# Kernel optimization log

Hardware: AMD Instinct MI355X
Metric: run time of the kernel (lower is better)

The kernel has to match this reference:

```python
import jax, jax.numpy as jnp
import numpy as np

B, S, HIDDEN = 4, 2048, 1024
NUM_EXPERTS = 8
TOP_K = 4
EPS = 1e-6


def setup_inputs() -> dict:
    key = jax.random.key(0)
    k0, k1, k2 = jax.random.split(key, 3)
    x = jax.random.normal(k0, (B, S, HIDDEN), dtype=jnp.float32)
    Wg = jax.random.normal(k1, (HIDDEN, NUM_EXPERTS), dtype=jnp.float32) * 0.02
    bg = jnp.zeros((NUM_EXPERTS,), dtype=jnp.float32)
    W = jax.random.normal(k2, (NUM_EXPERTS, HIDDEN, HIDDEN), dtype=jnp.float32) * 0.02
    b = jnp.zeros((NUM_EXPERTS, HIDDEN), dtype=jnp.float32)
    return {"x": x, "Wg": Wg, "bg": bg, "W": W, "b": b}


def reference(x, Wg, bg, W, b):
    Bb, Ss, D = x.shape
    xf = x.reshape(-1, D)                       # [T, D]
    T = xf.shape[0]

    # --- router ---
    router_logits = xf @ Wg + bg                # [T, E]
    router_probs = jax.nn.softmax(router_logits, axis=-1)
    top_k_probs, top_k_indices = jax.lax.top_k(router_probs, TOP_K)  # [T, K]
    top_k_weights = top_k_probs / (top_k_probs.sum(axis=-1, keepdims=True) + EPS)
    expert_mask = jax.nn.one_hot(top_k_indices, NUM_EXPERTS, dtype=jnp.float32).sum(axis=1)  # [T, E]

    # --- experts: original computes every expert on every token then masks;
    # same math expressed as one batched GEMM + gather ---
    all_out = jnp.einsum('td,edf->etf', xf, W) + b[:, None, :]  # [E, T, D]
    sel = all_out[top_k_indices.T, jnp.arange(T)[None, :]]      # [K, T, D]
    moe_output = jnp.einsum('tk,ktd->td', top_k_weights, sel).reshape(Bb, Ss, D)

    # --- load-balancing aux loss ---
    aux_loss = jnp.dot(expert_mask.mean(axis=0), router_probs.mean(axis=0)) * NUM_EXPERTS
    return moe_output, aux_loss
```

## Files before the change

kernel.cpp:

```cpp
#include <hip/hip_runtime.h>
#include <hip/hip_bf16.h>

#define T_TOK 8192
#define DH    1024
#define NE    8
#define TK    4

typedef unsigned short u16;
typedef __bf16 bf16x8 __attribute__((ext_vector_type(8)));
typedef float  f32x4  __attribute__((ext_vector_type(4)));

__device__ __forceinline__ u16 f2b(float f) {
    union { float f; unsigned u; } v; v.f = f;
    unsigned u = v.u;
    u += 0x7FFFu + ((u >> 16) & 1u);
    return (u16)(u >> 16);
}
__device__ __forceinline__ float b2f(u16 h) {
    union { unsigned u; float f; } v; v.u = ((unsigned)h) << 16;
    return v.f;
}
__device__ __forceinline__ void glds16(const u16* g, u16* l) {
    __builtin_amdgcn_global_load_lds((const __attribute__((address_space(1))) void*)g,
                                     (__attribute__((address_space(3))) void*)l, 16, 0, 0);
}

__global__ __launch_bounds__(256) void cast_w_kernel(const float* __restrict__ W,
                                                     u16* __restrict__ wbt) {
    __shared__ float tile[64][65];
    const int e  = blockIdx.z;
    const int d0 = blockIdx.y * 64;
    const int f0 = blockIdx.x * 64;
    const int r  = threadIdx.x >> 4;
    const int c4 = (threadIdx.x & 15) * 4;
    const float* src = W + ((size_t)e << 20) + (size_t)d0 * DH + f0;
    #pragma unroll
    for (int i = 0; i < 4; i++) {
        const int row = i * 16 + r;
        const float4 v = *(const float4*)(src + (size_t)row * DH + c4);
        tile[row][c4]     = v.x;
        tile[row][c4 + 1] = v.y;
        tile[row][c4 + 2] = v.z;
        tile[row][c4 + 3] = v.w;
    }
    __syncthreads();
    u16* dst = wbt + ((size_t)e << 20) + (size_t)f0 * DH + d0;
    #pragma unroll
    for (int i = 0; i < 4; i++) {
        const int orow = i * 16 + r;
        ushort4 o;
        o.x = f2b(tile[c4][orow]);
        o.y = f2b(tile[c4 + 1][orow]);
        o.z = f2b(tile[c4 + 2][orow]);
        o.w = f2b(tile[c4 + 3][orow]);
        *(ushort4*)(dst + (size_t)orow * DH + c4) = o;
    }
}

__global__ __launch_bounds__(512) void router_kernel(
    const float* __restrict__ x, const float* __restrict__ Wg, const float* __restrict__ bg,
    u16* __restrict__ xb,
    int* __restrict__ bucket_tok, float* __restrict__ bucket_w,
    int* __restrict__ tk_e, float* __restrict__ tk_w,
    int* __restrict__ cnt, float* __restrict__ probsum)
{
    __shared__ int   lcnt[NE];
    __shared__ float lprob[NE];
    __shared__ int   gbase[NE];
    const int tid = threadIdx.x;
    const int wv = tid >> 6, lane = tid & 63;
    const int t = blockIdx.x * 8 + wv;
    if (tid < NE) { lcnt[tid] = 0; lprob[tid] = 0.f; }
    __syncthreads();

    float a[NE] = {};
    {
        const float* xr = x + (size_t)t * DH;
        u16* xbr = xb + (size_t)t * DH;
        #pragma unroll
        for (int it = 0; it < 4; it++) {
            const int d = it * 256 + lane * 4;
            const float4 v = *(const float4*)(xr + d);
            ushort4 o;
            o.x = f2b(v.x); o.y = f2b(v.y); o.z = f2b(v.z); o.w = f2b(v.w);
            *(ushort4*)(xbr + d) = o;
            const float* wr = Wg + d * NE;
            #pragma unroll
            for (int e = 0; e < NE; e++)
                a[e] += v.x * wr[e] + v.y * wr[NE + e] + v.z * wr[2 * NE + e] + v.w * wr[3 * NE + e];
        }
    }
    #pragma unroll
    for (int e = 0; e < NE; e++) {
        float v = a[e];
        #pragma unroll
        for (int off = 32; off > 0; off >>= 1) v += __shfl_down(v, off);
        a[e] = v;
    }

    int idx4[TK]; float w4[TK]; int off4[TK];
    if (lane == 0) {
        float logits[NE], probs[NE];
        float mx = -1e30f;
        #pragma unroll
        for (int e = 0; e < NE; e++) { logits[e] = a[e] + bg[e]; mx = fmaxf(mx, logits[e]); }
        float Z = 0.f;
        #pragma unroll
        for (int e = 0; e < NE; e++) { probs[e] = expf(logits[e] - mx); Z += probs[e]; }
        const float rZ = 1.f / Z;
        #pragma unroll
        for (int e = 0; e < NE; e++) probs[e] *= rZ;

        float rem2[NE];
        #pragma unroll
        for (int e = 0; e < NE; e++) rem2[e] = probs[e];
        float s4 = 0.f;
        #pragma unroll
        for (int k = 0; k < TK; k++) {
            int best = 0; float bv = rem2[0];
            #pragma unroll
            for (int e = 1; e < NE; e++) if (rem2[e] > bv) { bv = rem2[e]; best = e; }
            idx4[k] = best; w4[k] = bv; s4 += bv; rem2[best] = -1e30f;
        }
        const float rs = 1.f / (s4 + 1e-6f);
        #pragma unroll
        for (int k = 0; k < TK; k++) {
            w4[k] *= rs;
            tk_e[t * TK + k] = idx4[k];
            tk_w[t * TK + k] = w4[k];
            off4[k] = atomicAdd(&lcnt[idx4[k]], 1);
        }
        #pragma unroll
        for (int e = 0; e < NE; e++) atomicAdd(&lprob[e], probs[e]);
    }
    __syncthreads();
    if (tid < NE) {
        gbase[tid] = atomicAdd(&cnt[tid], lcnt[tid]);
        atomicAdd(&probsum[tid], lprob[tid]);
    }
    __syncthreads();
    if (lane == 0) {
        #pragma unroll
        for (int k = 0; k < TK; k++) {
            const int e = idx4[k];
            const int slot = gbase[e] + off4[k];
            bucket_tok[e * T_TOK + slot] = (t << 2) | k;
            bucket_w[e * T_TOK + slot]   = w4[k];
        }
    }
}

__global__ __launch_bounds__(256) void moe_gemm_kernel(
    const u16* __restrict__ xb, const u16* __restrict__ wbt,
    const int* __restrict__ bucket_tok, const float* __restrict__ bucket_w,
    const int* __restrict__ cnt, u16* __restrict__ y)
{
    const int e  = blockIdx.z;
    const int M  = cnt[e];
    const int m0 = blockIdx.y * 128;
    if (m0 >= M) return;
    const int n0 = blockIdx.x * 128;

    __shared__ u16 As[128 * 32];
    __shared__ u16 Bs[128 * 32];
    __shared__ int   s_tok[128];
    __shared__ float s_w[128];

    const int tid  = threadIdx.x;
    const int lane = tid & 63;
    const int wave = tid >> 6;

    if (tid < 128) {
        const int slot = m0 + tid;
        if (slot < M) {
            s_tok[tid] = bucket_tok[e * T_TOK + slot];
            s_w[tid]   = bucket_w[e * T_TOK + slot];
        } else { s_tok[tid] = -1; s_w[tid] = 0.f; }
    }
    __syncthreads();

    const int l4 = lane >> 2;
    const int c8 = (lane & 3) * 8;
    const int r0 = (2 * wave) * 16 + l4;
    const int r1 = r0 + 16;
    const int t0 = s_tok[r0], t1 = s_tok[r1];
    const u16* gA0 = xb + (size_t)(t0 >= 0 ? (t0 >> 2) : 0) * DH + c8;
    const u16* gA1 = xb + (size_t)(t1 >= 0 ? (t1 >> 2) : 0) * DH + c8;
    const u16* gB0 = wbt + ((size_t)e << 20) + (size_t)(n0 + r0) * DH + c8;
    const u16* gB1 = gB0 + (size_t)16 * DH;
    u16* lA0 = &As[(2 * wave)     * 512];
    u16* lA1 = &As[(2 * wave + 1) * 512];
    u16* lB0 = &Bs[(2 * wave)     * 512];
    u16* lB1 = &Bs[(2 * wave + 1) * 512];

    const int mrow = (wave >> 1) * 64;
    const int ncol = (wave & 1) * 64;
    const int fr   = lane & 15;
    const int fq   = (lane >> 4) * 8;

    f32x4 acc[4][4] = {};

    for (int k0 = 0; k0 < DH; k0 += 32) {
        glds16(gA0 + k0, lA0);
        glds16(gA1 + k0, lA1);
        glds16(gB0 + k0, lB0);
        glds16(gB1 + k0, lB1);
        __syncthreads();
        bf16x8 af[4], bfv[4];
        #pragma unroll
        for (int i = 0; i < 4; i++)
            af[i] = *(const bf16x8*)&As[(mrow + i * 16 + fr) * 32 + fq];
        #pragma unroll
        for (int j = 0; j < 4; j++)
            bfv[j] = *(const bf16x8*)&Bs[(ncol + j * 16 + fr) * 32 + fq];
        #pragma unroll
        for (int i = 0; i < 4; i++)
            #pragma unroll
            for (int j = 0; j < 4; j++)
                acc[i][j] = __builtin_amdgcn_mfma_f32_16x16x32_bf16(af[i], bfv[j], acc[i][j], 0, 0, 0);
        __syncthreads();
    }

    const int cl = lane & 15;
    const int rb = (lane >> 4) * 4;
    #pragma unroll
    for (int i = 0; i < 4; i++) {
        #pragma unroll
        for (int r = 0; r < 4; r++) {
            const int srow = mrow + i * 16 + rb + r;
            const int tok = s_tok[srow];
            if (tok < 0) continue;
            const float w = s_w[srow];
            u16* yr = y + (size_t)tok * DH + (n0 + ncol + cl);
            #pragma unroll
            for (int j = 0; j < 4; j++)
                yr[j * 16] = f2b(acc[i][j][r] * w);
        }
    }
}

__global__ __launch_bounds__(256) void combine_kernel(
    const u16* __restrict__ y, const int* __restrict__ tk_e, const float* __restrict__ tk_w,
    const float* __restrict__ bexp,
    const int* __restrict__ cnt, const float* __restrict__ probsum,
    float* __restrict__ out, float* __restrict__ out_aux)
{
    const int t = blockIdx.x;
    const int c = threadIdx.x * 4;
    if (t == 0 && threadIdx.x == 0) {
        float s = 0.f;
        for (int e = 0; e < NE; e++) s += (float)cnt[e] * probsum[e];
        out_aux[0] = s * (float)NE / ((float)T_TOK * (float)T_TOK);
    }
    float o0 = 0.f, o1 = 0.f, o2 = 0.f, o3 = 0.f;
    #pragma unroll
    for (int k = 0; k < TK; k++) {
        const int e   = tk_e[t * TK + k];
        const float w = tk_w[t * TK + k];
        const ushort4 yv = *(const ushort4*)(y + ((size_t)(t * TK + k)) * DH + c);
        const float4  bv = *(const float4*)(bexp + (size_t)e * DH + c);
        o0 += b2f(yv.x) + w * bv.x;
        o1 += b2f(yv.y) + w * bv.y;
        o2 += b2f(yv.z) + w * bv.z;
        o3 += b2f(yv.w) + w * bv.w;
    }
    float4 ov = {o0, o1, o2, o3};
    *(float4*)(out + (size_t)t * DH + c) = ov;
}

extern "C" void kernel_launch(void* const* d_in, const int* in_sizes, int n_in,
                              void* d_out, int out_size, void* d_ws, size_t ws_size,
                              hipStream_t stream)
{
    const float* x  = (const float*)d_in[0];
    const float* Wg = (const float*)d_in[1];
    const float* bg = (const float*)d_in[2];
    const float* W  = (const float*)d_in[3];
    const float* b  = (const float*)d_in[4];
    float* out = (float*)d_out;

    char* ws = (char*)d_ws;
    u16*   xb         = (u16*)(ws);
    u16*   wbt        = (u16*)(ws + 16777216);
    u16*   y          = (u16*)(ws + 33554432);
    int*   bucket_tok = (int*)(ws + 100663296);
    float* bucket_w   = (float*)(ws + 100925440);
    int*   tk_e       = (int*)(ws + 101187584);
    float* tk_w       = (float*)(ws + 101318656);
    int*   cnt        = (int*)(ws + 101449728);
    float* probsum    = (float*)(ws + 101449760);

    hipMemsetAsync(cnt, 0, 64, stream);

    cast_w_kernel<<<dim3(16, 16, NE), 256, 0, stream>>>(W, wbt);
    router_kernel<<<1024, 512, 0, stream>>>(x, Wg, bg, xb, bucket_tok, bucket_w, tk_e, tk_w, cnt, probsum);
    moe_gemm_kernel<<<dim3(8, 64, NE), 256, 0, stream>>>(xb, wbt, bucket_tok, bucket_w, cnt, y);
    combine_kernel<<<8192, 256, 0, stream>>>(y, tk_e, tk_w, b, cnt, probsum, out, out + (size_t)T_TOK * DH);
}
```

Before: 259.8 us.

## Double-buffer LDS tiles in MoE GEMM with async prefetch two stages ahead

```diff
diff --git a/kernel.cpp b/kernel.cpp
--- a/kernel.cpp
+++ b/kernel.cpp
@@ -24,6 +24,9 @@
     __builtin_amdgcn_global_load_lds((const __attribute__((address_space(1))) void*)g,
                                      (__attribute__((address_space(3))) void*)l, 16, 0, 0);
 }
+
+#define FENCE() asm volatile("" ::: "memory")
+#define SBAR()  do { FENCE(); __builtin_amdgcn_s_barrier(); FENCE(); } while (0)
 
 __global__ __launch_bounds__(256) void cast_w_kernel(const float* __restrict__ W,
                                                      u16* __restrict__ wbt) {
@@ -161,8 +164,8 @@
     if (m0 >= M) return;
     const int n0 = blockIdx.x * 128;
 
-    __shared__ u16 As[128 * 32];
-    __shared__ u16 Bs[128 * 32];
+    __shared__ u16 As[2][128 * 32];
+    __shared__ u16 Bs[2][128 * 32];
     __shared__ int   s_tok[128];
     __shared__ float s_w[128];
 
@@ -188,10 +191,7 @@
     const u16* gA1 = xb + (size_t)(t1 >= 0 ? (t1 >> 2) : 0) * DH + c8;
     const u16* gB0 = wbt + ((size_t)e << 20) + (size_t)(n0 + r0) * DH + c8;
     const u16* gB1 = gB0 + (size_t)16 * DH;
-    u16* lA0 = &As[(2 * wave)     * 512];
-    u16* lA1 = &As[(2 * wave + 1) * 512];
-    u16* lB0 = &Bs[(2 * wave)     * 512];
-    u16* lB1 = &Bs[(2 * wave + 1) * 512];
+    const int chunk = (2 * wave) * 512;
 
     const int mrow = (wave >> 1) * 64;
     const int ncol = (wave & 1) * 64;
@@ -200,25 +200,39 @@
 
     f32x4 acc[4][4] = {};
 
-    for (int k0 = 0; k0 < DH; k0 += 32) {
-        glds16(gA0 + k0, lA0);
-        glds16(gA1 + k0, lA1);
-        glds16(gB0 + k0, lB0);
-        glds16(gB1 + k0, lB1);
-        __syncthreads();
+    auto stage = [&](int kt) {
+        const int b  = kt & 1;
+        const int ko = kt * 32;
+        glds16(gA0 + ko, &As[b][chunk]);
+        glds16(gA1 + ko, &As[b][chunk + 512]);
+        glds16(gB0 + ko, &Bs[b][chunk]);
+        glds16(gB1 + ko, &Bs[b][chunk + 512]);
+    };
+
+    stage(0); stage(1);
+    asm volatile("s_waitcnt vmcnt(4)" ::: "memory");
+    SBAR();
+
+    for (int t = 0; t < 32; ++t) {
+        const int b = t & 1;
         bf16x8 af[4], bfv[4];
         #pragma unroll
         for (int i = 0; i < 4; i++)
-            af[i] = *(const bf16x8*)&As[(mrow + i * 16 + fr) * 32 + fq];
+            af[i] = *(const bf16x8*)&As[b][(mrow + i * 16 + fr) * 32 + fq];
         #pragma unroll
         for (int j = 0; j < 4; j++)
-            bfv[j] = *(const bf16x8*)&Bs[(ncol + j * 16 + fr) * 32 + fq];
+            bfv[j] = *(const bf16x8*)&Bs[b][(ncol + j * 16 + fr) * 32 + fq];
+        asm volatile("s_waitcnt lgkmcnt(0)" ::: "memory");
+        SBAR();
+        if (t + 2 < 32) stage(t + 2);
         #pragma unroll
         for (int i = 0; i < 4; i++)
             #pragma unroll
             for (int j = 0; j < 4; j++)
                 acc[i][j] = __builtin_amdgcn_mfma_f32_16x16x32_bf16(af[i], bfv[j], acc[i][j], 0, 0, 0);
-        __syncthreads();
+        if (t < 30)       asm volatile("s_waitcnt vmcnt(4)" ::: "memory");
+        else if (t == 30) asm volatile("s_waitcnt vmcnt(0)" ::: "memory");
+        if (t < 31) SBAR();
     }
 
     const int cl = lane & 15;
```

New measurement: 259.2 us. About the same (-0.3%).

## Rewrite expert GEMM as persistent 256x256 double-buffered swizzled pipeline

Applied to the files above, without the earlier changes.

```diff
diff --git a/kernel.cpp b/kernel.cpp
--- a/kernel.cpp
+++ b/kernel.cpp
@@ -24,6 +24,11 @@
     __builtin_amdgcn_global_load_lds((const __attribute__((address_space(1))) void*)g,
                                      (__attribute__((address_space(3))) void*)l, 16, 0, 0);
 }
+
+#define FENCE() asm volatile("" ::: "memory")
+#define SBAR()  do { FENCE(); __builtin_amdgcn_s_barrier(); FENCE(); } while (0)
+#define WAITLGKM0() do { asm volatile("s_waitcnt lgkmcnt(0)" ::: "memory"); \
+                         __builtin_amdgcn_sched_barrier(0); } while (0)
 
 __global__ __launch_bounds__(256) void cast_w_kernel(const float* __restrict__ W,
                                                      u16* __restrict__ wbt) {
@@ -150,91 +155,170 @@
     }
 }
 
-__global__ __launch_bounds__(256) void moe_gemm_kernel(
+__global__ __launch_bounds__(512, 2) void moe_gemm_kernel(
     const u16* __restrict__ xb, const u16* __restrict__ wbt,
     const int* __restrict__ bucket_tok, const float* __restrict__ bucket_w,
     const int* __restrict__ cnt, u16* __restrict__ y)
 {
-    const int e  = blockIdx.z;
-    const int M  = cnt[e];
-    const int m0 = blockIdx.y * 128;
-    if (m0 >= M) return;
-    const int n0 = blockIdx.x * 128;
-
-    __shared__ u16 As[128 * 32];
-    __shared__ u16 Bs[128 * 32];
-    __shared__ int   s_tok[128];
-    __shared__ float s_w[128];
+    __shared__ u16 As[2][256 * 64];
+    __shared__ u16 Bs[2][256 * 64];
+    __shared__ int   s_tok[256];
+    __shared__ float s_w[256];
 
     const int tid  = threadIdx.x;
     const int lane = tid & 63;
-    const int wave = tid >> 6;
-
-    if (tid < 128) {
-        const int slot = m0 + tid;
-        if (slot < M) {
-            s_tok[tid] = bucket_tok[e * T_TOK + slot];
-            s_w[tid]   = bucket_w[e * T_TOK + slot];
-        } else { s_tok[tid] = -1; s_w[tid] = 0.f; }
-    }
-    __syncthreads();
-
-    const int l4 = lane >> 2;
-    const int c8 = (lane & 3) * 8;
-    const int r0 = (2 * wave) * 16 + l4;
-    const int r1 = r0 + 16;
-    const int t0 = s_tok[r0], t1 = s_tok[r1];
-    const u16* gA0 = xb + (size_t)(t0 >= 0 ? (t0 >> 2) : 0) * DH + c8;
-    const u16* gA1 = xb + (size_t)(t1 >= 0 ? (t1 >> 2) : 0) * DH + c8;
-    const u16* gB0 = wbt + ((size_t)e << 20) + (size_t)(n0 + r0) * DH + c8;
-    const u16* gB1 = gB0 + (size_t)16 * DH;
-    u16* lA0 = &As[(2 * wave)     * 512];
-    u16* lA1 = &As[(2 * wave + 1) * 512];
-    u16* lB0 = &Bs[(2 * wave)     * 512];
-    u16* lB1 = &Bs[(2 * wave + 1) * 512];
-
-    const int mrow = (wave >> 1) * 64;
-    const int ncol = (wave & 1) * 64;
+    const int wid  = tid >> 6;
+    const int wr   = wid >> 2;
+    const int wc   = wid & 3;
     const int fr   = lane & 15;
     const int fq   = (lane >> 4) * 8;
-
-    f32x4 acc[4][4] = {};
-
-    for (int k0 = 0; k0 < DH; k0 += 32) {
-        glds16(gA0 + k0, lA0);
-        glds16(gA1 + k0, lA1);
-        glds16(gB0 + k0, lB0);
-        glds16(gB1 + k0, lB1);
+    const int swz  = (fr & 7) << 3;
+    const int gsw  = ((lane & 7) ^ (lane >> 3)) * 8;
+    const int crow = lane >> 3;
+
+    for (int vt = blockIdx.x; vt < 1024; vt += 256) {
+        const int mb = vt >> 5;
+        const int e  = (vt >> 2) & 7;
+        const int nb = vt & 3;
+        const int M  = cnt[e];
+        const int m0 = mb << 8;
+        if (m0 >= M) continue;
+        const int n0 = nb << 8;
+
         __syncthreads();
-        bf16x8 af[4], bfv[4];
-        #pragma unroll
-        for (int i = 0; i < 4; i++)
-            af[i] = *(const bf16x8*)&As[(mrow + i * 16 + fr) * 32 + fq];
-        #pragma unroll
-        for (int j = 0; j < 4; j++)
-            bfv[j] = *(const bf16x8*)&Bs[(ncol + j * 16 + fr) * 32 + fq];
-        #pragma unroll
-        for (int i = 0; i < 4; i++)
-            #pragma unroll
-            for (int j = 0; j < 4; j++)
-                acc[i][j] = __builtin_amdgcn_mfma_f32_16x16x32_bf16(af[i], bfv[j], acc[i][j], 0, 0, 0);
+        if (tid < 256) {
+            const int slot = m0 + tid;
+            if (slot < M) {
+                s_tok[tid] = bucket_tok[e * T_TOK + slot];
+                s_w[tid]   = bucket_w[e * T_TOK + slot];
+            } else { s_tok[tid] = -1; s_w[tid] = 0.f; }
+        }
         __syncthreads();
-    }
-
-    const int cl = lane & 15;
-    const int rb = (lane >> 4) * 4;
-    #pragma unroll
-    for (int i = 0; i < 4; i++) {
-        #pragma unroll
-        for (int r = 0; r < 4; r++) {
-            const int srow = mrow + i * 16 + rb + r;
-            const int tok = s_tok[srow];
-            if (tok < 0) continue;
-            const float w = s_w[srow];
-            u16* yr = y + (size_t)tok * DH + (n0 + ncol + cl);
-            #pragma unroll
-            for (int j = 0; j < 4; j++)
-                yr[j * 16] = f2b(acc[i][j][r] * w);
+
+        const u16* gA[4]; const u16* gB[4];
+        #pragma unroll
+        for (int q = 0; q < 4; q++) {
+            const int row = wid * 32 + q * 8 + crow;
+            const int tok = s_tok[row];
+            gA[q] = xb + (size_t)(tok >= 0 ? (tok >> 2) : 0) * DH + gsw;
+            gB[q] = wbt + ((size_t)e << 20) + (size_t)(n0 + row) * DH + gsw;
+        }
+
+        f32x4 acc[8][4] = {};
+
+        auto STAGE = [&](int kt) {
+            const int p  = kt & 1;
+            const int ko = kt * 64;
+            #pragma unroll
+            for (int q = 0; q < 4; q++)
+                glds16(gA[q] + ko, &As[p][(wid * 4 + q) * 512]);
+            #pragma unroll
+            for (int q = 0; q < 4; q++)
+                glds16(gB[q] + ko, &Bs[p][(wid * 4 + q) * 512]);
+        };
+
+        STAGE(0); STAGE(1);
+        asm volatile("s_waitcnt vmcnt(8)" ::: "memory");
+        SBAR();
+
+        const int arow = (wr * 128 + fr) * 64;
+        const int brow = (wc * 64  + fr) * 64;
+        const int c0 = fq ^ swz;
+        const int c1 = (32 + fq) ^ swz;
+
+        bf16x8 afL[4][2], afH[4][2], bfL[2][2], bfH[2][2];
+
+        for (int kt = 0; kt < 16; ++kt) {
+            const int p = kt & 1;
+            const u16* Ap = &As[p][0];
+            const u16* Bp = &Bs[p][0];
+
+            #pragma unroll
+            for (int mi = 0; mi < 4; mi++) {
+                afL[mi][0] = *(const bf16x8*)&Ap[arow + mi * 1024 + c0];
+                afL[mi][1] = *(const bf16x8*)&Ap[arow + mi * 1024 + c1];
+            }
+            #pragma unroll
+            for (int nj = 0; nj < 2; nj++) {
+                bfL[nj][0] = *(const bf16x8*)&Bp[brow + nj * 1024 + c0];
+                bfL[nj][1] = *(const bf16x8*)&Bp[brow + nj * 1024 + c1];
+            }
+            SBAR(); WAITLGKM0();
+            __builtin_amdgcn_s_setprio(1);
+            #pragma unroll
+            for (int mi = 0; mi < 4; mi++)
+                #pragma unroll
+                for (int nj = 0; nj < 2; nj++) {
+                    acc[mi][nj] = __builtin_amdgcn_mfma_f32_16x16x32_bf16(afL[mi][0], bfL[nj][0], acc[mi][nj], 0, 0, 0);
+                    acc[mi][nj] = __builtin_amdgcn_mfma_f32_16x16x32_bf16(afL[mi][1], bfL[nj][1], acc[mi][nj], 0, 0, 0);
+                }
+            __builtin_amdgcn_s_setprio(0);
+            SBAR();
+
+            #pragma unroll
+            for (int nj = 0; nj < 2; nj++) {
+                bfH[nj][0] = *(const bf16x8*)&Bp[brow + (nj + 2) * 1024 + c0];
+                bfH[nj][1] = *(const bf16x8*)&Bp[brow + (nj + 2) * 1024 + c1];
+            }
+            SBAR(); WAITLGKM0();
+            __builtin_amdgcn_s_setprio(1);
+            #pragma unroll
+            for (int mi = 0; mi < 4; mi++)
+                #pragma unroll
+                for (int nj = 0; nj < 2; nj++) {
+                    acc[mi][nj + 2] = __builtin_amdgcn_mfma_f32_16x16x32_bf16(afL[mi][0], bfH[nj][0], acc[mi][nj + 2], 0, 0, 0);
+                    acc[mi][nj + 2] = __builtin_amdgcn_mfma_f32_16x16x32_bf16(afL[mi][1], bfH[nj][1], acc[mi][nj + 2], 0, 0, 0);
+                }
+            __builtin_amdgcn_s_setprio(0);
+            SBAR();
+
+            #pragma unroll
+            for (int mi = 0; mi < 4; mi++) {
+                afH[mi][0] = *(const bf16x8*)&Ap[arow + (mi + 4) * 1024 + c0];
+                afH[mi][1] = *(const bf16x8*)&Ap[arow + (mi + 4) * 1024 + c1];
+            }
+            SBAR(); WAITLGKM0();
+            __builtin_amdgcn_s_setprio(1);
+            #pragma unroll
+            for (int mi = 0; mi < 4; mi++)
+                #pragma unroll
+                for (int nj = 0; nj < 2; nj++) {
+                    acc[mi + 4][nj + 2] = __builtin_amdgcn_mfma_f32_16x16x32_bf16(afH[mi][0], bfH[nj][0], acc[mi + 4][nj + 2], 0, 0, 0);
+                    acc[mi + 4][nj + 2] = __builtin_amdgcn_mfma_f32_16x16x32_bf16(afH[mi][1], bfH[nj][1], acc[mi + 4][nj + 2], 0, 0, 0);
+                }
+            __builtin_amdgcn_s_setprio(0);
+            SBAR();
+
+            if (kt < 14) STAGE(kt + 2);
+            __builtin_amdgcn_s_setprio(1);
+            #pragma unroll
+            for (int mi = 0; mi < 4; mi++)
+                #pragma unroll
+                for (int nj = 0; nj < 2; nj++) {
+                    acc[mi + 4][nj] = __builtin_amdgcn_mfma_f32_16x16x32_bf16(afH[mi][0], bfL[nj][0], acc[mi + 4][nj], 0, 0, 0);
+                    acc[mi + 4][nj] = __builtin_amdgcn_mfma_f32_16x16x32_bf16(afH[mi][1], bfL[nj][1], acc[mi + 4][nj], 0, 0, 0);
+                }
+            __builtin_amdgcn_s_setprio(0);
+            if (kt < 14)       asm volatile("s_waitcnt vmcnt(8)" ::: "memory");
+            else if (kt == 14) asm volatile("s_waitcnt vmcnt(0)" ::: "memory");
+            SBAR();
+        }
+
+        const int cl = lane & 15;
+        const int rb = (lane >> 4) * 4;
+        #pragma unroll
+        for (int mi = 0; mi < 8; mi++) {
+            #pragma unroll
+            for (int r = 0; r < 4; r++) {
+                const int srow = wr * 128 + mi * 16 + rb + r;
+                const int tok = s_tok[srow];
+                if (tok < 0) continue;
+                const float w = s_w[srow];
+                u16* yr = y + (size_t)tok * DH + (n0 + wc * 64 + cl);
+                #pragma unroll
+                for (int nj = 0; nj < 4; nj++)
+                    yr[nj * 16] = f2b(acc[mi][nj][r] * w);
+            }
         }
     }
 }
@@ -294,6 +378,6 @@
 
     cast_w_kernel<<<dim3(16, 16, NE), 256, 0, stream>>>(W, wbt);
     router_kernel<<<1024, 512, 0, stream>>>(x, Wg, bg, xb, bucket_tok, bucket_w, tk_e, tk_w, cnt, probsum);
-    moe_gemm_kernel<<<dim3(8, 64, NE), 256, 0, stream>>>(xb, wbt, bucket_tok, bucket_w, cnt, y);
+    moe_gemm_kernel<<<dim3(256), 512, 0, stream>>>(xb, wbt, bucket_tok, bucket_w, cnt, y);
     combine_kernel<<<8192, 256, 0, stream>>>(y, tk_e, tk_w, b, cnt, probsum, out, out + (size_t)T_TOK * DH);
 }
```

Measured after the change: 267.3 us. 1.03x slower.
